# Kernel tuning notes

Hardware: AMD Instinct MI355X
Metric: run time of the kernel (lower is better)

The kernel has to match this reference:

```python
import jax, jax.numpy as jnp
import numpy as np

NPOINT = 1024
RADIUS = 0.2
NSAMPLE = 32


def setup_inputs() -> dict:
    key = jax.random.key(0)
    ks = jax.random.split(key, 8)
    B, N, C = 8, 8192, 64
    xyz = jax.random.uniform(ks[0], (B, N, 3), dtype=jnp.float32)
    features = jax.random.normal(ks[1], (B, N, C), dtype=jnp.float32)
    c_in = C + 3  # QueryAndGroup concatenates relative xyz with features
    s = 0.05
    w1 = jax.random.normal(ks[2], (c_in, 64), dtype=jnp.float32) * s
    b1 = jnp.zeros((64,), jnp.float32)
    w2 = jax.random.normal(ks[3], (64, 64), dtype=jnp.float32) * s
    b2 = jnp.zeros((64,), jnp.float32)
    w3 = jax.random.normal(ks[4], (64, 128), dtype=jnp.float32) * s
    b3 = jnp.zeros((128,), jnp.float32)
    return {"xyz": xyz, "features": features, "w1": w1, "b1": b1,
            "w2": w2, "b2": b2, "w3": w3, "b3": b3}


def farthest_point_sample(xyz, npoint):
    # xyz: (B, N, 3) -> (B, npoint) int32 indices
    B, N, _ = xyz.shape

    def step(carry, _):
        dist, far = carry
        centroid = jnp.take_along_axis(xyz, far[:, None, None], axis=1)  # (B,1,3)
        d = jnp.sum((xyz - centroid) ** 2, axis=-1)  # (B,N)
        dist = jnp.minimum(dist, d)
        nxt = jnp.argmax(dist, axis=-1).astype(jnp.int32)
        return (dist, nxt), far

    init = (jnp.full((B, N), 1e10, jnp.float32), jnp.zeros((B,), jnp.int32))
    _, idxs = jax.lax.scan(step, init, None, length=npoint)
    return idxs.T  # (B, npoint)


def ball_query(radius, nsample, xyz, new_xyz):
    # returns (B, S, nsample) int32 neighbor indices into N
    sq = jnp.sum((new_xyz[:, :, None, :] - xyz[:, None, :, :]) ** 2, axis=-1)  # (B,S,N)
    B, S, N = sq.shape
    idx = jnp.broadcast_to(jnp.arange(N, dtype=jnp.int32), (B, S, N))
    idx = jnp.where(sq > radius * radius, N, idx)
    idx = jnp.sort(idx, axis=-1)[:, :, :nsample]
    first = idx[:, :, :1]
    idx = jnp.where(idx == N, first, idx)  # pad with first valid index
    return idx


_gather = jax.vmap(lambda pts, idx: pts[idx])  # per-batch fancy gather


def reference(xyz, features, w1, b1, w2, b2, w3, b3):
    fps_idx = farthest_point_sample(xyz, NPOINT)
    new_xyz = _gather(xyz, fps_idx)  # (B, S, 3)
    nbr_idx = ball_query(RADIUS, NSAMPLE, xyz, new_xyz)  # (B, S, K)
    g_xyz = _gather(xyz, nbr_idx) - new_xyz[:, :, None, :]  # (B,S,K,3) relative coords
    g_feat = _gather(features, nbr_idx)  # (B, S, K, C)
    x = jnp.concatenate([g_xyz, g_feat], axis=-1)  # (B, S, K, C+3)
    # shared pointwise MLP (Conv2d 1x1 + ReLU)
    x = jax.nn.relu(x @ w1 + b1)
    x = jax.nn.relu(x @ w2 + b2)
    x = jax.nn.relu(x @ w3 + b3)
    new_features = jnp.max(x, axis=2)  # max-pool over neighbors -> (B, S, 128)
    return new_xyz, jnp.transpose(new_features, (0, 2, 1))  # (B,S,3), (B,128,S)
```

## Files before the change

### kernel.cpp

```cpp
#include <hip/hip_runtime.h>
#include <stdint.h>

#define N_PTS 8192
#define B_SZ 8
#define NPOINT_ 1024
#define NSAMPLE_ 32

typedef float __attribute__((ext_vector_type(2))) f32x2;

template <int CTRL>
__device__ __forceinline__ float dpp_maxf(float v) {
    int o = __builtin_amdgcn_update_dpp(__float_as_int(v), __float_as_int(v),
                                        CTRL, 0xf, 0xf, false);
    return fmaxf(v, __int_as_float(o));
}
template <int CTRL>
__device__ __forceinline__ int dpp_mini(int v) {
    int o = __builtin_amdgcn_update_dpp(v, v, CTRL, 0xf, 0xf, false);
    return (o < v) ? o : v;
}

__global__ __launch_bounds__(512) void fps_kernel(const float* __restrict__ xyz,
                                                  float* __restrict__ new_xyz) {
    __shared__ float4 spts[N_PTS];
    __shared__ float  cval[2][8];
    __shared__ int    cidx[2][8];
    const int b = blockIdx.x;
    const int t = threadIdx.x;
    const float* bx = xyz + (size_t)b * N_PTS * 3;

    f32x2 px[8], py[8], pz[8], dst[8];
#pragma unroll
    for (int jj = 0; jj < 8; ++jj) {
        int p0 = t + 512 * (2 * jj);
        int p1 = t + 512 * (2 * jj + 1);
        float x0 = bx[3 * p0 + 0], y0 = bx[3 * p0 + 1], z0 = bx[3 * p0 + 2];
        float x1 = bx[3 * p1 + 0], y1 = bx[3 * p1 + 1], z1 = bx[3 * p1 + 2];
        spts[p0] = make_float4(x0, y0, z0, 0.0f);
        spts[p1] = make_float4(x1, y1, z1, 0.0f);
        px[jj] = f32x2{x0, x1}; py[jj] = f32x2{y0, y1}; pz[jj] = f32x2{z0, z1};
        dst[jj] = f32x2{1e10f, 1e10f};
    }
    __syncthreads();

    float cx = bx[0], cy = bx[1], cz = bx[2];
    if (t == 0) {
        new_xyz[(b * NPOINT_) * 3 + 0] = cx;
        new_xyz[(b * NPOINT_) * 3 + 1] = cy;
        new_xyz[(b * NPOINT_) * 3 + 2] = cz;
    }
    const int wave = t >> 6, lane = t & 63;

    for (int it = 1; it < NPOINT_; ++it) {
        f32x2 cx2 = f32x2{cx, cx}, cy2 = f32x2{cy, cy}, cz2 = f32x2{cz, cz};
        {
#pragma clang fp contract(off)
#pragma unroll
            for (int jj = 0; jj < 8; ++jj) {
                f32x2 dx = px[jj] - cx2;
                f32x2 dy = py[jj] - cy2;
                f32x2 dz = pz[jj] - cz2;
                f32x2 d  = (dx * dx + dy * dy) + dz * dz;
                dst[jj] = __builtin_elementwise_min(dst[jj], d);
            }
        }
        f32x2 m01 = __builtin_elementwise_max(dst[0], dst[1]);
        f32x2 m23 = __builtin_elementwise_max(dst[2], dst[3]);
        f32x2 m45 = __builtin_elementwise_max(dst[4], dst[5]);
        f32x2 m67 = __builtin_elementwise_max(dst[6], dst[7]);
        f32x2 m03 = __builtin_elementwise_max(m01, m23);
        f32x2 m47 = __builtin_elementwise_max(m45, m67);
        f32x2 mm  = __builtin_elementwise_max(m03, m47);
        float bv  = fmaxf(mm.x, mm.y);
        int lj = 0;
#pragma unroll
        for (int jj = 7; jj >= 0; --jj) {
            lj = (dst[jj].y == bv) ? 2 * jj + 1 : lj;
            lj = (dst[jj].x == bv) ? 2 * jj     : lj;
        }
        int idx = (lj << 9) + t;

        float mv = bv;
        mv = dpp_maxf<0x111>(mv);
        mv = dpp_maxf<0x112>(mv);
        mv = dpp_maxf<0x114>(mv);
        mv = dpp_maxf<0x118>(mv);
        mv = dpp_maxf<0x142>(mv);
        mv = dpp_maxf<0x143>(mv);
        float wmax = __int_as_float(__builtin_amdgcn_readlane(__float_as_int(mv), 63));
        int ic = (bv == wmax) ? idx : 0x7FFFFFFF;
        ic = dpp_mini<0x111>(ic);
        ic = dpp_mini<0x112>(ic);
        ic = dpp_mini<0x114>(ic);
        ic = dpp_mini<0x118>(ic);
        ic = dpp_mini<0x142>(ic);
        ic = dpp_mini<0x143>(ic);

        const int buf = it & 1;
        if (lane == 63) { cval[buf][wave] = wmax; cidx[buf][wave] = ic; }
        __syncthreads();

        float cv = cval[buf][lane & 7];
        int   ci = cidx[buf][lane & 7];
        float gm = cv;
        gm = dpp_maxf<0x111>(gm);
        gm = dpp_maxf<0x112>(gm);
        gm = dpp_maxf<0x114>(gm);
        float gmax = __int_as_float(__builtin_amdgcn_readlane(__float_as_int(gm), 7));
        int ic2 = (cv == gmax) ? ci : 0x7FFFFFFF;
        ic2 = dpp_mini<0x111>(ic2);
        ic2 = dpp_mini<0x112>(ic2);
        ic2 = dpp_mini<0x114>(ic2);
        int wi = __builtin_amdgcn_readlane(ic2, 7);

        float4 sp = spts[wi];
        cx = sp.x; cy = sp.y; cz = sp.z;
        if (t == 0) {
            new_xyz[(b * NPOINT_ + it) * 3 + 0] = cx;
            new_xyz[(b * NPOINT_ + it) * 3 + 1] = cy;
            new_xyz[(b * NPOINT_ + it) * 3 + 2] = cz;
        }
    }
}

__global__ __launch_bounds__(512) void ballquery_kernel(const float* __restrict__ xyz,
                                                        const float* __restrict__ new_xyz,
                                                        int* __restrict__ nbr_idx) {
    __shared__ float sx[N_PTS], sy[N_PTS], sz[N_PTS];
    const int b     = blockIdx.x >> 4;
    const int chunk = blockIdx.x & 15;
    const int t = threadIdx.x;
    const float* bx = xyz + (size_t)b * N_PTS * 3;
    for (int p = t; p < N_PTS; p += 512) {
        sx[p] = bx[3 * p + 0];
        sy[p] = bx[3 * p + 1];
        sz[p] = bx[3 * p + 2];
    }
    __syncthreads();
    const int wave = t >> 6, lane = t & 63;
    const float r2 = 0.04f;

    for (int si = 0; si < 8; ++si) {
        int s = chunk * 64 + wave * 8 + si;
        int g = b * NPOINT_ + s;
        float cx = new_xyz[g * 3 + 0];
        float cy = new_xyz[g * 3 + 1];
        float cz = new_xyz[g * 3 + 2];
        int taken = 0;
        int firstIdx = -1;
        int* ob = nbr_idx + (size_t)g * NSAMPLE_;
        for (int c = 0; c < N_PTS / 64 && taken < NSAMPLE_; ++c) {
            int p = c * 64 + lane;
            float dx = __fsub_rn(sx[p], cx);
            float dy = __fsub_rn(sy[p], cy);
            float dz = __fsub_rn(sz[p], cz);
            float sq = __fadd_rn(__fadd_rn(__fmul_rn(dx, dx), __fmul_rn(dy, dy)),
                                 __fmul_rn(dz, dz));
            bool pred = !(sq > r2);
            unsigned long long mask = __ballot(pred);
            if (mask) {
                int cnt = __popcll(mask);
                if (firstIdx < 0) firstIdx = c * 64 + (__ffsll(mask) - 1);
                if (pred) {
                    int pos = taken + __popcll(mask & ((1ull << lane) - 1ull));
                    if (pos < NSAMPLE_) ob[pos] = p;
                }
                taken += cnt;
            }
        }
        if (lane >= taken && lane < NSAMPLE_) ob[lane] = firstIdx;
    }
}

__global__ __launch_bounds__(512, 2) void mlp_kernel(const float* __restrict__ xyz,
                                                     const float* __restrict__ feat,
                                                     const float* __restrict__ new_xyz,
                                                     const int* __restrict__ nbr_idx,
                                                     const float* __restrict__ w1,
                                                     const float* __restrict__ b1,
                                                     const float* __restrict__ w2,
                                                     const float* __restrict__ b2,
                                                     const float* __restrict__ w3,
                                                     const float* __restrict__ b3,
                                                     float* __restrict__ out) {
    __shared__ float lw1T[64 * 68];
    __shared__ float lb1[64];
    __shared__ float lw2T[64 * 64];
    __shared__ float lb2[64];
    __shared__ float lw3T[128 * 64];
    __shared__ float lb3[128];
    __shared__ float xb[8][16 * 68];
    __shared__ float hb[8][16 * 68];

    const int t = threadIdx.x;
    for (int i = t; i < 67 * 64; i += 512) { int k = i >> 6, c = i & 63; lw1T[c * 68 + k] = w1[i]; }
    if (t < 64) lw1T[t * 68 + 67] = 0.0f;
    for (int i = t; i < 64 * 64; i += 512)  { int k = i >> 6, c = i & 63;  lw2T[c * 64 + k] = w2[i]; }
    for (int i = t; i < 64 * 128; i += 512) { int k = i >> 7, c = i & 127; lw3T[c * 64 + k] = w3[i]; }
    if (t < 64)  { lb1[t] = b1[t]; lb2[t] = b2[t]; }
    if (t < 128) lb3[t] = b3[t];
    __syncthreads();

    const int wave = t >> 6, lane = t & 63;
    float* xw = xb[wave];
    float* hw = hb[wave];
    const float* wc1 = lw1T + lane * 68;
    const float* wc2 = lw2T + lane * 64;
    const float* wca = lw3T + lane * 64;
    const float* wcb = lw3T + (lane + 64) * 64;

    for (int g = blockIdx.x * 8 + wave; g < B_SZ * NPOINT_; g += gridDim.x * 8) {
        const int b = g >> 10, s = g & 1023;
        const float cx = new_xyz[g * 3 + 0];
        const float cy = new_xyz[g * 3 + 1];
        const float cz = new_xyz[g * 3 + 2];
        float mo0 = 0.0f, mo1 = 0.0f;

        for (int half = 0; half < 2; ++half) {
            int iis[16];
#pragma unroll
            for (int r = 0; r < 16; ++r)
                iis[r] = nbr_idx[(size_t)g * NSAMPLE_ + half * 16 + r];
#pragma unroll
            for (int r = 0; r < 16; ++r) {
                xw[r * 68 + 3 + lane] = feat[((size_t)b * N_PTS + iis[r]) * 64 + lane];
                if (lane < 3) {
                    float pv = xyz[((size_t)b * N_PTS + iis[r]) * 3 + lane];
                    float cv = (lane == 0) ? cx : ((lane == 1) ? cy : cz);
                    xw[r * 68 + lane] = pv - cv;
                }
                if (lane == 0) xw[r * 68 + 67] = 0.0f;
            }
            f32x2 acc2[16];
            {
                float bias = lb1[lane];
#pragma unroll
                for (int r = 0; r < 16; ++r) acc2[r] = f32x2{bias, 0.0f};
                for (int kk = 0; kk < 68; kk += 4) {
                    f32x2 wA = *(const f32x2*)(wc1 + kk);
                    f32x2 wB = *(const f32x2*)(wc1 + kk + 2);
#pragma unroll
                    for (int r = 0; r < 16; ++r) {
                        float4 xv = *(const float4*)&xw[r * 68 + kk];
                        f32x2 xa = f32x2{xv.x, xv.y};
                        f32x2 xc = f32x2{xv.z, xv.w};
                        acc2[r] = xa * wA + acc2[r];
                        acc2[r] = xc * wB + acc2[r];
                    }
                }
#pragma unroll
                for (int r = 0; r < 16; ++r)
                    hw[r * 68 + lane] = fmaxf(acc2[r].x + acc2[r].y, 0.0f);
            }
            {
                float bias = lb2[lane];
#pragma unroll
                for (int r = 0; r < 16; ++r) acc2[r] = f32x2{bias, 0.0f};
                for (int kk = 0; kk < 64; kk += 4) {
                    f32x2 wA = *(const f32x2*)(wc2 + kk);
                    f32x2 wB = *(const f32x2*)(wc2 + kk + 2);
#pragma unroll
                    for (int r = 0; r < 16; ++r) {
                        float4 hv = *(const float4*)&hw[r * 68 + kk];
                        f32x2 xa = f32x2{hv.x, hv.y};
                        f32x2 xc = f32x2{hv.z, hv.w};
                        acc2[r] = xa * wA + acc2[r];
                        acc2[r] = xc * wB + acc2[r];
                    }
                }
#pragma unroll
                for (int r = 0; r < 16; ++r)
                    xw[r * 68 + lane] = fmaxf(acc2[r].x + acc2[r].y, 0.0f);
            }
            {
                f32x2 a2[16], c2[16];
                float bb0 = lb3[lane], bb1 = lb3[lane + 64];
#pragma unroll
                for (int r = 0; r < 16; ++r) { a2[r] = f32x2{bb0, 0.0f}; c2[r] = f32x2{bb1, 0.0f}; }
                for (int kk = 0; kk < 64; kk += 4) {
                    f32x2 wA0 = *(const f32x2*)(wca + kk);
                    f32x2 wB0 = *(const f32x2*)(wca + kk + 2);
                    f32x2 wA1 = *(const f32x2*)(wcb + kk);
                    f32x2 wB1 = *(const f32x2*)(wcb + kk + 2);
#pragma unroll
                    for (int r = 0; r < 16; ++r) {
                        float4 hv = *(const float4*)&xw[r * 68 + kk];
                        f32x2 xa = f32x2{hv.x, hv.y};
                        f32x2 xc = f32x2{hv.z, hv.w};
                        a2[r] = xa * wA0 + a2[r];
                        a2[r] = xc * wB0 + a2[r];
                        c2[r] = xa * wA1 + c2[r];
                        c2[r] = xc * wB1 + c2[r];
                    }
                }
#pragma unroll
                for (int r = 0; r < 16; ++r) {
                    mo0 = fmaxf(mo0, fmaxf(a2[r].x + a2[r].y, 0.0f));
                    mo1 = fmaxf(mo1, fmaxf(c2[r].x + c2[r].y, 0.0f));
                }
            }
        }
        out[((size_t)b * 128 + lane) * 1024 + s]      = mo0;
        out[((size_t)b * 128 + lane + 64) * 1024 + s] = mo1;
    }
}

extern "C" void kernel_launch(void* const* d_in, const int* in_sizes, int n_in,
                              void* d_out, int out_size, void* d_ws, size_t ws_size,
                              hipStream_t stream) {
    const float* xyz  = (const float*)d_in[0];
    const float* feat = (const float*)d_in[1];
    const float* w1   = (const float*)d_in[2];
    const float* b1   = (const float*)d_in[3];
    const float* w2   = (const float*)d_in[4];
    const float* b2   = (const float*)d_in[5];
    const float* w3   = (const float*)d_in[6];
    const float* b3   = (const float*)d_in[7];

    float* out_xyz  = (float*)d_out;
    float* out_feat = (float*)d_out + B_SZ * NPOINT_ * 3;
    int*   nbr      = (int*)d_ws;

    fps_kernel<<<B_SZ, 512, 0, stream>>>(xyz, out_xyz);
    ballquery_kernel<<<B_SZ * 16, 512, 0, stream>>>(xyz, out_xyz, nbr);
    mlp_kernel<<<256, 512, 0, stream>>>(xyz, feat, out_xyz, nbr,
                                        w1, b1, w2, b2, w3, b3, out_feat);
}
```

Baseline: 1.234 ms.

## Fuse FPS, ball query and MLP into one producer-consumer persistent kernel

Replaces the three launches with one kernel. Eight producer blocks run farthest-point sampling and publish a progress counter every 64 centroids, while consumer blocks spin-wait on that counter and then run the ball query and MLP per centroid. This overlaps the serial FPS with the downstream work and drops the neighbor-index round trip through global memory. In exchange, ball query now reads xyz from global memory instead of LDS. Correctness depends on all producer blocks being co-resident with the consumers, otherwise the spin-wait can deadlock.

Measured after the change: 1.026 ms. 16.9% less time.

```diff
diff --git a/kernel.cpp b/kernel.cpp
--- a/kernel.cpp
+++ b/kernel.cpp
@@ -5,6 +5,10 @@
 #define B_SZ 8
 #define NPOINT_ 1024
 #define NSAMPLE_ 32
+#define NPROD 8
+#define NCONS 240
+#define CWAVES (NCONS * 8)
+#define PUBK 64
 
 typedef float __attribute__((ext_vector_type(2))) f32x2;
 
@@ -20,309 +24,347 @@
     return (o < v) ? o : v;
 }
 
-__global__ __launch_bounds__(512) void fps_kernel(const float* __restrict__ xyz,
-                                                  float* __restrict__ new_xyz) {
-    __shared__ float4 spts[N_PTS];
-    __shared__ float  cval[2][8];
-    __shared__ int    cidx[2][8];
-    const int b = blockIdx.x;
+__device__ __forceinline__ float ld_coh(const float* p) {
+    return __int_as_float(__hip_atomic_load((int*)p, __ATOMIC_RELAXED,
+                                            __HIP_MEMORY_SCOPE_AGENT));
+}
+__device__ __forceinline__ void st_coh(float* p, float v) {
+    __hip_atomic_store((int*)p, __float_as_int(v), __ATOMIC_RELAXED,
+                       __HIP_MEMORY_SCOPE_AGENT);
+}
+
+#define SM_SPTS 0
+#define SM_CVAL 131072
+#define SM_CIDX 131136
+#define SM_W1 0
+#define SM_W2 17408
+#define SM_W3 33792
+#define SM_B1 66560
+#define SM_B2 66816
+#define SM_B3 67072
+#define SM_XB 67584
+#define SM_HB 102400
+#define SM_NIDX 137216
+#define SM_TOTAL 138240
+
+__global__ __launch_bounds__(512, 2) void fused_kernel(
+    const float* __restrict__ xyz, const float* __restrict__ feat,
+    const float* __restrict__ w1, const float* __restrict__ b1,
+    const float* __restrict__ w2, const float* __restrict__ b2,
+    const float* __restrict__ w3, const float* __restrict__ b3,
+    float* __restrict__ new_xyz, float* __restrict__ out,
+    int* __restrict__ prog) {
+    __shared__ __align__(16) char smem[SM_TOTAL];
     const int t = threadIdx.x;
-    const float* bx = xyz + (size_t)b * N_PTS * 3;
-
-    f32x2 px[8], py[8], pz[8], dst[8];
-#pragma unroll
-    for (int jj = 0; jj < 8; ++jj) {
-        int p0 = t + 512 * (2 * jj);
-        int p1 = t + 512 * (2 * jj + 1);
-        float x0 = bx[3 * p0 + 0], y0 = bx[3 * p0 + 1], z0 = bx[3 * p0 + 2];
-        float x1 = bx[3 * p1 + 0], y1 = bx[3 * p1 + 1], z1 = bx[3 * p1 + 2];
-        spts[p0] = make_float4(x0, y0, z0, 0.0f);
-        spts[p1] = make_float4(x1, y1, z1, 0.0f);
-        px[jj] = f32x2{x0, x1}; py[jj] = f32x2{y0, y1}; pz[jj] = f32x2{z0, z1};
-        dst[jj] = f32x2{1e10f, 1e10f};
+    const int wave = t >> 6, lane = t & 63;
+
+    if (blockIdx.x < NPROD) {
+        float4* spts = (float4*)smem;
+        float* cval = (float*)(smem + SM_CVAL);
+        int* cidx = (int*)(smem + SM_CIDX);
+        const int b = blockIdx.x;
+        const float* bx = xyz + (size_t)b * N_PTS * 3;
+        int* pp = prog + b * 64;
+
+        f32x2 px[8], py[8], pz[8], dst[8];
+#pragma unroll
+        for (int jj = 0; jj < 8; ++jj) {
+            int p0 = t + 512 * (2 * jj);
+            int p1 = t + 512 * (2 * jj + 1);
+            float x0 = bx[3 * p0 + 0], y0 = bx[3 * p0 + 1], z0 = bx[3 * p0 + 2];
+            float x1 = bx[3 * p1 + 0], y1 = bx[3 * p1 + 1], z1 = bx[3 * p1 + 2];
+            spts[p0] = make_float4(x0, y0, z0, 0.0f);
+            spts[p1] = make_float4(x1, y1, z1, 0.0f);
+            px[jj] = f32x2{x0, x1};
+            py[jj] = f32x2{y0, y1};
+            pz[jj] = f32x2{z0, z1};
+            dst[jj] = f32x2{1e10f, 1e10f};
+        }
+        __syncthreads();
+
+        float cx = bx[0], cy = bx[1], cz = bx[2];
+        if (t == 0) {
+            st_coh(&new_xyz[(b * NPOINT_) * 3 + 0], cx);
+            st_coh(&new_xyz[(b * NPOINT_) * 3 + 1], cy);
+            st_coh(&new_xyz[(b * NPOINT_) * 3 + 2], cz);
+        }
+
+        for (int it = 1; it < NPOINT_; ++it) {
+            f32x2 cx2 = f32x2{cx, cx}, cy2 = f32x2{cy, cy}, cz2 = f32x2{cz, cz};
+            {
+#pragma clang fp contract(off)
+#pragma unroll
+                for (int jj = 0; jj < 8; ++jj) {
+                    f32x2 dx = px[jj] - cx2;
+                    f32x2 dy = py[jj] - cy2;
+                    f32x2 dz = pz[jj] - cz2;
+                    f32x2 d = (dx * dx + dy * dy) + dz * dz;
+                    dst[jj] = __builtin_elementwise_min(dst[jj], d);
+                }
+            }
+            f32x2 m01 = __builtin_elementwise_max(dst[0], dst[1]);
+            f32x2 m23 = __builtin_elementwise_max(dst[2], dst[3]);
+            f32x2 m45 = __builtin_elementwise_max(dst[4], dst[5]);
+            f32x2 m67 = __builtin_elementwise_max(dst[6], dst[7]);
+            f32x2 m03 = __builtin_elementwise_max(m01, m23);
+            f32x2 m47 = __builtin_elementwise_max(m45, m67);
+            f32x2 mm = __builtin_elementwise_max(m03, m47);
+            float bv = fmaxf(mm.x, mm.y);
+            int lj = 0;
+#pragma unroll
+            for (int jj = 7; jj >= 0; --jj) {
+                lj = (dst[jj].y == bv) ? 2 * jj + 1 : lj;
+                lj = (dst[jj].x == bv) ? 2 * jj : lj;
+            }
+            int idx = (lj << 9) + t;
+
+            float mv = bv;
+            mv = dpp_maxf<0x111>(mv);
+            mv = dpp_maxf<0x112>(mv);
+            mv = dpp_maxf<0x114>(mv);
+            mv = dpp_maxf<0x118>(mv);
+            mv = dpp_maxf<0x142>(mv);
+            mv = dpp_maxf<0x143>(mv);
+            float wmax = __int_as_float(
+                __builtin_amdgcn_readlane(__float_as_int(mv), 63));
+            int ic = (bv == wmax) ? idx : 0x7FFFFFFF;
+            ic = dpp_mini<0x111>(ic);
+            ic = dpp_mini<0x112>(ic);
+            ic = dpp_mini<0x114>(ic);
+            ic = dpp_mini<0x118>(ic);
+            ic = dpp_mini<0x142>(ic);
+            ic = dpp_mini<0x143>(ic);
+
+            const int buf = it & 1;
+            if (lane == 63) {
+                cval[buf * 8 + wave] = wmax;
+                cidx[buf * 8 + wave] = ic;
+            }
+            __syncthreads();
+
+            float cv = cval[buf * 8 + (lane & 7)];
+            int ci = cidx[buf * 8 + (lane & 7)];
+            float gm = cv;
+            gm = dpp_maxf<0x111>(gm);
+            gm = dpp_maxf<0x112>(gm);
+            gm = dpp_maxf<0x114>(gm);
+            float gmax =
+                __int_as_float(__builtin_amdgcn_readlane(__float_as_int(gm), 7));
+            int ic2 = (cv == gmax) ? ci : 0x7FFFFFFF;
+            ic2 = dpp_mini<0x111>(ic2);
+            ic2 = dpp_mini<0x112>(ic2);
+            ic2 = dpp_mini<0x114>(ic2);
+            int wi = __builtin_amdgcn_readlane(ic2, 7);
+
+            float4 sp = spts[wi];
+            cx = sp.x;
+            cy = sp.y;
+            cz = sp.z;
+            if (t == 0) {
+                st_coh(&new_xyz[(b * NPOINT_ + it) * 3 + 0], cx);
+                st_coh(&new_xyz[(b * NPOINT_ + it) * 3 + 1], cy);
+                st_coh(&new_xyz[(b * NPOINT_ + it) * 3 + 2], cz);
+                if ((it & (PUBK - 1)) == (PUBK - 1)) {
+                    __hip_atomic_store(pp, it + 1, __ATOMIC_RELEASE,
+                                       __HIP_MEMORY_SCOPE_AGENT);
+                }
+            }
+        }
+    } else {
+        float* lw1T = (float*)(smem + SM_W1);
+        float* lw2T = (float*)(smem + SM_W2);
+        float* lw3T = (float*)(smem + SM_W3);
+        float* lb1 = (float*)(smem + SM_B1);
+        float* lb2 = (float*)(smem + SM_B2);
+        float* lb3 = (float*)(smem + SM_B3);
+
+        for (int i = t; i < 67 * 64; i += 512) {
+            int k = i >> 6, c = i & 63;
+            lw1T[c * 68 + k] = w1[i];
+        }
+        if (t < 64) lw1T[t * 68 + 67] = 0.0f;
+        for (int i = t; i < 64 * 64; i += 512) {
+            int k = i >> 6, c = i & 63;
+            lw2T[c * 64 + k] = w2[i];
+        }
+        for (int i = t; i < 64 * 128; i += 512) {
+            int k = i >> 7, c = i & 127;
+            lw3T[c * 64 + k] = w3[i];
+        }
+        if (t < 64) {
+            lb1[t] = b1[t];
+            lb2[t] = b2[t];
+        }
+        if (t < 128) lb3[t] = b3[t];
+        __syncthreads();
+
+        float* xw = (float*)(smem + SM_XB) + wave * (16 * 68);
+        float* hw = (float*)(smem + SM_HB) + wave * (16 * 68);
+        int* nw = (int*)(smem + SM_NIDX) + wave * 32;
+        const float* wc1 = lw1T + lane * 68;
+        const float* wc2 = lw2T + lane * 64;
+        const float* wca = lw3T + lane * 64;
+        const float* wcb = lw3T + (lane + 64) * 64;
+
+        const int widx = (blockIdx.x - NPROD) * 8 + wave;
+        for (int cc = widx; cc < B_SZ * NPOINT_; cc += CWAVES) {
+            const int s = cc >> 3, b = cc & 7;
+            const int g = (b << 10) + s;
+            int* pp = prog + b * 64;
+
+            int pv = __hip_atomic_load(pp, __ATOMIC_RELAXED,
+                                       __HIP_MEMORY_SCOPE_AGENT);
+            while (pv <= s) {
+                if (s - pv >= 64)
+                    __builtin_amdgcn_s_sleep(64);
+                else
+                    __builtin_amdgcn_s_sleep(16);
+                pv = __hip_atomic_load(pp, __ATOMIC_RELAXED,
+                                       __HIP_MEMORY_SCOPE_AGENT);
+            }
+            __builtin_amdgcn_fence(__ATOMIC_ACQUIRE, "agent");
+            const float cx = ld_coh(&new_xyz[g * 3 + 0]);
+            const float cy = ld_coh(&new_xyz[g * 3 + 1]);
+            const float cz = ld_coh(&new_xyz[g * 3 + 2]);
+
+            const float* bx = xyz + (size_t)b * N_PTS * 3;
+            const float r2 = 0.04f;
+            int taken = 0, firstIdx = -1;
+            for (int ch = 0; ch < N_PTS / 64 && taken < NSAMPLE_; ++ch) {
+                int p = ch * 64 + lane;
+                float dxq = __fsub_rn(bx[3 * p + 0], cx);
+                float dyq = __fsub_rn(bx[3 * p + 1], cy);
+                float dzq = __fsub_rn(bx[3 * p + 2], cz);
+                float sq = __fadd_rn(
+                    __fadd_rn(__fmul_rn(dxq, dxq), __fmul_rn(dyq, dyq)),
+                    __fmul_rn(dzq, dzq));
+                bool pred = !(sq > r2);
+                unsigned long long mask = __ballot(pred);
+                if (mask) {
+                    int cnt = __popcll(mask);
+                    if (firstIdx < 0) firstIdx = ch * 64 + (__ffsll(mask) - 1);
+                    if (pred) {
+                        int pos =
+                            taken + __popcll(mask & ((1ull << lane) - 1ull));
+                        if (pos < NSAMPLE_) nw[pos] = p;
+                    }
+                    taken += cnt;
+                }
+            }
+            if (lane >= taken && lane < NSAMPLE_) nw[lane] = firstIdx;
+            asm volatile("s_waitcnt lgkmcnt(0)" ::: "memory");
+
+            float mo0 = 0.0f, mo1 = 0.0f;
+            for (int half = 0; half < 2; ++half) {
+                int iis[16];
+#pragma unroll
+                for (int r = 0; r < 16; ++r) iis[r] = nw[half * 16 + r];
+#pragma unroll
+                for (int r = 0; r < 16; ++r) {
+                    xw[r * 68 + 3 + lane] =
+                        feat[((size_t)b * N_PTS + iis[r]) * 64 + lane];
+                    if (lane < 3) {
+                        float pv2 = xyz[((size_t)b * N_PTS + iis[r]) * 3 + lane];
+                        float cv = (lane == 0) ? cx : ((lane == 1) ? cy : cz);
+                        xw[r * 68 + lane] = pv2 - cv;
+                    }
+                    if (lane == 0) xw[r * 68 + 67] = 0.0f;
+                }
+                f32x2 acc2[16];
+                {
+                    float bias = lb1[lane];
+#pragma unroll
+                    for (int r = 0; r < 16; ++r) acc2[r] = f32x2{bias, 0.0f};
+                    for (int kk = 0; kk < 68; kk += 4) {
+                        f32x2 wA = *(const f32x2*)(wc1 + kk);
+                        f32x2 wB = *(const f32x2*)(wc1 + kk + 2);
+#pragma unroll
+                        for (int r = 0; r < 16; ++r) {
+                            float4 xv = *(const float4*)&xw[r * 68 + kk];
+                            f32x2 xa = f32x2{xv.x, xv.y};
+                            f32x2 xc = f32x2{xv.z, xv.w};
+                            acc2[r] = xa * wA + acc2[r];
+                            acc2[r] = xc * wB + acc2[r];
+                        }
+                    }
+#pragma unroll
+                    for (int r = 0; r < 16; ++r)
+                        hw[r * 68 + lane] = fmaxf(acc2[r].x + acc2[r].y, 0.0f);
+                }
+                {
+                    float bias = lb2[lane];
+#pragma unroll
+                    for (int r = 0; r < 16; ++r) acc2[r] = f32x2{bias, 0.0f};
+                    for (int kk = 0; kk < 64; kk += 4) {
+                        f32x2 wA = *(const f32x2*)(wc2 + kk);
+                        f32x2 wB = *(const f32x2*)(wc2 + kk + 2);
+#pragma unroll
+                        for (int r = 0; r < 16; ++r) {
+                            float4 hv = *(const float4*)&hw[r * 68 + kk];
+                            f32x2 xa = f32x2{hv.x, hv.y};
+                            f32x2 xc = f32x2{hv.z, hv.w};
+                            acc2[r] = xa * wA + acc2[r];
+                            acc2[r] = xc * wB + acc2[r];
+                        }
+                    }
+#pragma unroll
+                    for (int r = 0; r < 16; ++r)
+                        xw[r * 68 + lane] = fmaxf(acc2[r].x + acc2[r].y, 0.0f);
+                }
+                {
+                    f32x2 a2[16], c2[16];
+                    float bb0 = lb3[lane], bb1 = lb3[lane + 64];
+#pragma unroll
+                    for (int r = 0; r < 16; ++r) {
+                        a2[r] = f32x2{bb0, 0.0f};
+                        c2[r] = f32x2{bb1, 0.0f};
+                    }
+                    for (int kk = 0; kk < 64; kk += 4) {
+                        f32x2 wA0 = *(const f32x2*)(wca + kk);
+                        f32x2 wB0 = *(const f32x2*)(wca + kk + 2);
+                        f32x2 wA1 = *(const f32x2*)(wcb + kk);
+                        f32x2 wB1 = *(const f32x2*)(wcb + kk + 2);
+#pragma unroll
+                        for (int r = 0; r < 16; ++r) {
+                            float4 hv = *(const float4*)&xw[r * 68 + kk];
+                            f32x2 xa = f32x2{hv.x, hv.y};
+                            f32x2 xc = f32x2{hv.z, hv.w};
+                            a2[r] = xa * wA0 + a2[r];
+                            a2[r] = xc * wB0 + a2[r];
+                            c2[r] = xa * wA1 + c2[r];
+                            c2[r] = xc * wB1 + c2[r];
+                        }
+                    }
+#pragma unroll
+                    for (int r = 0; r < 16; ++r) {
+                        mo0 = fmaxf(mo0, fmaxf(a2[r].x + a2[r].y, 0.0f));
+                        mo1 = fmaxf(mo1, fmaxf(c2[r].x + c2[r].y, 0.0f));
+                    }
+                }
+            }
+            out[((size_t)b * 128 + lane) * 1024 + s] = mo0;
+            out[((size_t)b * 128 + lane + 64) * 1024 + s] = mo1;
+        }
     }
-    __syncthreads();
-
-    float cx = bx[0], cy = bx[1], cz = bx[2];
-    if (t == 0) {
-        new_xyz[(b * NPOINT_) * 3 + 0] = cx;
-        new_xyz[(b * NPOINT_) * 3 + 1] = cy;
-        new_xyz[(b * NPOINT_) * 3 + 2] = cz;
-    }
-    const int wave = t >> 6, lane = t & 63;
-
-    for (int it = 1; it < NPOINT_; ++it) {
-        f32x2 cx2 = f32x2{cx, cx}, cy2 = f32x2{cy, cy}, cz2 = f32x2{cz, cz};
-        {
-#pragma clang fp contract(off)
-#pragma unroll
-            for (int jj = 0; jj < 8; ++jj) {
-                f32x2 dx = px[jj] - cx2;
-                f32x2 dy = py[jj] - cy2;
-                f32x2 dz = pz[jj] - cz2;
-                f32x2 d  = (dx * dx + dy * dy) + dz * dz;
-                dst[jj] = __builtin_elementwise_min(dst[jj], d);
-            }
-        }
-        f32x2 m01 = __builtin_elementwise_max(dst[0], dst[1]);
-        f32x2 m23 = __builtin_elementwise_max(dst[2], dst[3]);
-        f32x2 m45 = __builtin_elementwise_max(dst[4], dst[5]);
-        f32x2 m67 = __builtin_elementwise_max(dst[6], dst[7]);
-        f32x2 m03 = __builtin_elementwise_max(m01, m23);
-        f32x2 m47 = __builtin_elementwise_max(m45, m67);
-        f32x2 mm  = __builtin_elementwise_max(m03, m47);
-        float bv  = fmaxf(mm.x, mm.y);
-        int lj = 0;
-#pragma unroll
-        for (int jj = 7; jj >= 0; --jj) {
-            lj = (dst[jj].y == bv) ? 2 * jj + 1 : lj;
-            lj = (dst[jj].x == bv) ? 2 * jj     : lj;
-        }
-        int idx = (lj << 9) + t;
-
-        float mv = bv;
-        mv = dpp_maxf<0x111>(mv);
-        mv = dpp_maxf<0x112>(mv);
-        mv = dpp_maxf<0x114>(mv);
-        mv = dpp_maxf<0x118>(mv);
-        mv = dpp_maxf<0x142>(mv);
-        mv = dpp_maxf<0x143>(mv);
-        float wmax = __int_as_float(__builtin_amdgcn_readlane(__float_as_int(mv), 63));
-        int ic = (bv == wmax) ? idx : 0x7FFFFFFF;
-        ic = dpp_mini<0x111>(ic);
-        ic = dpp_mini<0x112>(ic);
-        ic = dpp_mini<0x114>(ic);
-        ic = dpp_mini<0x118>(ic);
-        ic = dpp_mini<0x142>(ic);
-        ic = dpp_mini<0x143>(ic);
-
-        const int buf = it & 1;
-        if (lane == 63) { cval[buf][wave] = wmax; cidx[buf][wave] = ic; }
-        __syncthreads();
-
-        float cv = cval[buf][lane & 7];
-        int   ci = cidx[buf][lane & 7];
-        float gm = cv;
-        gm = dpp_maxf<0x111>(gm);
-        gm = dpp_maxf<0x112>(gm);
-        gm = dpp_maxf<0x114>(gm);
-        float gmax = __int_as_float(__builtin_amdgcn_readlane(__float_as_int(gm), 7));
-        int ic2 = (cv == gmax) ? ci : 0x7FFFFFFF;
-        ic2 = dpp_mini<0x111>(ic2);
-        ic2 = dpp_mini<0x112>(ic2);
-        ic2 = dpp_mini<0x114>(ic2);
-        int wi = __builtin_amdgcn_readlane(ic2, 7);
-
-        float4 sp = spts[wi];
-        cx = sp.x; cy = sp.y; cz = sp.z;
-        if (t == 0) {
-            new_xyz[(b * NPOINT_ + it) * 3 + 0] = cx;
-            new_xyz[(b * NPOINT_ + it) * 3 + 1] = cy;
-            new_xyz[(b * NPOINT_ + it) * 3 + 2] = cz;
-        }
-    }
-}
-
-__global__ __launch_bounds__(512) void ballquery_kernel(const float* __restrict__ xyz,
-                                                        const float* __restrict__ new_xyz,
-                                                        int* __restrict__ nbr_idx) {
-    __shared__ float sx[N_PTS], sy[N_PTS], sz[N_PTS];
-    const int b     = blockIdx.x >> 4;
-    const int chunk = blockIdx.x & 15;
-    const int t = threadIdx.x;
-    const float* bx = xyz + (size_t)b * N_PTS * 3;
-    for (int p = t; p < N_PTS; p += 512) {
-        sx[p] = bx[3 * p + 0];
-        sy[p] = bx[3 * p + 1];
-        sz[p] = bx[3 * p + 2];
-    }
-    __syncthreads();
-    const int wave = t >> 6, lane = t & 63;
-    const float r2 = 0.04f;
-
-    for (int si = 0; si < 8; ++si) {
-        int s = chunk * 64 + wave * 8 + si;
-        int g = b * NPOINT_ + s;
-        float cx = new_xyz[g * 3 + 0];
-        float cy = new_xyz[g * 3 + 1];
-        float cz = new_xyz[g * 3 + 2];
-        int taken = 0;
-        int firstIdx = -1;
-        int* ob = nbr_idx + (size_t)g * NSAMPLE_;
-        for (int c = 0; c < N_PTS / 64 && taken < NSAMPLE_; ++c) {
-            int p = c * 64 + lane;
-            float dx = __fsub_rn(sx[p], cx);
-            float dy = __fsub_rn(sy[p], cy);
-            float dz = __fsub_rn(sz[p], cz);
-            float sq = __fadd_rn(__fadd_rn(__fmul_rn(dx, dx), __fmul_rn(dy, dy)),
-                                 __fmul_rn(dz, dz));
-            bool pred = !(sq > r2);
-            unsigned long long mask = __ballot(pred);
-            if (mask) {
-                int cnt = __popcll(mask);
-                if (firstIdx < 0) firstIdx = c * 64 + (__ffsll(mask) - 1);
-                if (pred) {
-                    int pos = taken + __popcll(mask & ((1ull << lane) - 1ull));
-                    if (pos < NSAMPLE_) ob[pos] = p;
-                }
-                taken += cnt;
-            }
-        }
-        if (lane >= taken && lane < NSAMPLE_) ob[lane] = firstIdx;
-    }
-}
-
-__global__ __launch_bounds__(512, 2) void mlp_kernel(const float* __restrict__ xyz,
-                                                     const float* __restrict__ feat,
-                                                     const float* __restrict__ new_xyz,
-                                                     const int* __restrict__ nbr_idx,
-                                                     const float* __restrict__ w1,
-                                                     const float* __restrict__ b1,
-                                                     const float* __restrict__ w2,
-                                                     const float* __restrict__ b2,
-                                                     const float* __restrict__ w3,
-                                                     const float* __restrict__ b3,
-                                                     float* __restrict__ out) {
-    __shared__ float lw1T[64 * 68];
-    __shared__ float lb1[64];
-    __shared__ float lw2T[64 * 64];
-    __shared__ float lb2[64];
-    __shared__ float lw3T[128 * 64];
-    __shared__ float lb3[128];
-    __shared__ float xb[8][16 * 68];
-    __shared__ float hb[8][16 * 68];
-
-    const int t = threadIdx.x;
-    for (int i = t; i < 67 * 64; i += 512) { int k = i >> 6, c = i & 63; lw1T[c * 68 + k] = w1[i]; }
-    if (t < 64) lw1T[t * 68 + 67] = 0.0f;
-    for (int i = t; i < 64 * 64; i += 512)  { int k = i >> 6, c = i & 63;  lw2T[c * 64 + k] = w2[i]; }
-    for (int i = t; i < 64 * 128; i += 512) { int k = i >> 7, c = i & 127; lw3T[c * 64 + k] = w3[i]; }
-    if (t < 64)  { lb1[t] = b1[t]; lb2[t] = b2[t]; }
-    if (t < 128) lb3[t] = b3[t];
-    __syncthreads();
-
-    const int wave = t >> 6, lane = t & 63;
-    float* xw = xb[wave];
-    float* hw = hb[wave];
-    const float* wc1 = lw1T + lane * 68;
-    const float* wc2 = lw2T + lane * 64;
-    const float* wca = lw3T + lane * 64;
-    const float* wcb = lw3T + (lane + 64) * 64;
-
-    for (int g = blockIdx.x * 8 + wave; g < B_SZ * NPOINT_; g += gridDim.x * 8) {
-        const int b = g >> 10, s = g & 1023;
-        const float cx = new_xyz[g * 3 + 0];
-        const float cy = new_xyz[g * 3 + 1];
-        const float cz = new_xyz[g * 3 + 2];
-        float mo0 = 0.0f, mo1 = 0.0f;
-
-        for (int half = 0; half < 2; ++half) {
-            int iis[16];
-#pragma unroll
-            for (int r = 0; r < 16; ++r)
-                iis[r] = nbr_idx[(size_t)g * NSAMPLE_ + half * 16 + r];
-#pragma unroll
-            for (int r = 0; r < 16; ++r) {
-                xw[r * 68 + 3 + lane] = feat[((size_t)b * N_PTS + iis[r]) * 64 + lane];
-                if (lane < 3) {
-                    float pv = xyz[((size_t)b * N_PTS + iis[r]) * 3 + lane];
-                    float cv = (lane == 0) ? cx : ((lane == 1) ? cy : cz);
-                    xw[r * 68 + lane] = pv - cv;
-                }
-                if (lane == 0) xw[r * 68 + 67] = 0.0f;
-            }
-            f32x2 acc2[16];
-            {
-                float bias = lb1[lane];
-#pragma unroll
-                for (int r = 0; r < 16; ++r) acc2[r] = f32x2{bias, 0.0f};
-                for (int kk = 0; kk < 68; kk += 4) {
-                    f32x2 wA = *(const f32x2*)(wc1 + kk);
-                    f32x2 wB = *(const f32x2*)(wc1 + kk + 2);
-#pragma unroll
-                    for (int r = 0; r < 16; ++r) {
-                        float4 xv = *(const float4*)&xw[r * 68 + kk];
-                        f32x2 xa = f32x2{xv.x, xv.y};
-                        f32x2 xc = f32x2{xv.z, xv.w};
-                        acc2[r] = xa * wA + acc2[r];
-                        acc2[r] = xc * wB + acc2[r];
-                    }
-                }
-#pragma unroll
-                for (int r = 0; r < 16; ++r)
-                    hw[r * 68 + lane] = fmaxf(acc2[r].x + acc2[r].y, 0.0f);
-            }
-            {
-                float bias = lb2[lane];
-#pragma unroll
-                for (int r = 0; r < 16; ++r) acc2[r] = f32x2{bias, 0.0f};
-                for (int kk = 0; kk < 64; kk += 4) {
-                    f32x2 wA = *(const f32x2*)(wc2 + kk);
-                    f32x2 wB = *(const f32x2*)(wc2 + kk + 2);
-#pragma unroll
-                    for (int r = 0; r < 16; ++r) {
-                        float4 hv = *(const float4*)&hw[r * 68 + kk];
-                        f32x2 xa = f32x2{hv.x, hv.y};
-                        f32x2 xc = f32x2{hv.z, hv.w};
-                        acc2[r] = xa * wA + acc2[r];
-                        acc2[r] = xc * wB + acc2[r];
-                    }
-                }
-#pragma unroll
-                for (int r = 0; r < 16; ++r)
-                    xw[r * 68 + lane] = fmaxf(acc2[r].x + acc2[r].y, 0.0f);
-            }
-            {
-                f32x2 a2[16], c2[16];
-                float bb0 = lb3[lane], bb1 = lb3[lane + 64];
-#pragma unroll
-                for (int r = 0; r < 16; ++r) { a2[r] = f32x2{bb0, 0.0f}; c2[r] = f32x2{bb1, 0.0f}; }
-                for (int kk = 0; kk < 64; kk += 4) {
-                    f32x2 wA0 = *(const f32x2*)(wca + kk);
-                    f32x2 wB0 = *(const f32x2*)(wca + kk + 2);
-                    f32x2 wA1 = *(const f32x2*)(wcb + kk);
-                    f32x2 wB1 = *(const f32x2*)(wcb + kk + 2);
-#pragma unroll
-                    for (int r = 0; r < 16; ++r) {
-                        float4 hv = *(const float4*)&xw[r * 68 + kk];
-                        f32x2 xa = f32x2{hv.x, hv.y};
-                        f32x2 xc = f32x2{hv.z, hv.w};
-                        a2[r] = xa * wA0 + a2[r];
-                        a2[r] = xc * wB0 + a2[r];
-                        c2[r] = xa * wA1 + c2[r];
-                        c2[r] = xc * wB1 + c2[r];
-                    }
-                }
-#pragma unroll
-                for (int r = 0; r < 16; ++r) {
-                    mo0 = fmaxf(mo0, fmaxf(a2[r].x + a2[r].y, 0.0f));
-                    mo1 = fmaxf(mo1, fmaxf(c2[r].x + c2[r].y, 0.0f));
-                }
-            }
-        }
-        out[((size_t)b * 128 + lane) * 1024 + s]      = mo0;
-        out[((size_t)b * 128 + lane + 64) * 1024 + s] = mo1;
-    }
 }
 
 extern "C" void kernel_launch(void* const* d_in, const int* in_sizes, int n_in,
-                              void* d_out, int out_size, void* d_ws, size_t ws_size,
-                              hipStream_t stream) {
-    const float* xyz  = (const float*)d_in[0];
+                              void* d_out, int out_size, void* d_ws,
+                              size_t ws_size, hipStream_t stream) {
+    const float* xyz = (const float*)d_in[0];
     const float* feat = (const float*)d_in[1];
-    const float* w1   = (const float*)d_in[2];
-    const float* b1   = (const float*)d_in[3];
-    const float* w2   = (const float*)d_in[4];
-    const float* b2   = (const float*)d_in[5];
-    const float* w3   = (const float*)d_in[6];
-    const float* b3   = (const float*)d_in[7];
-
-    float* out_xyz  = (float*)d_out;
+    const float* w1 = (const float*)d_in[2];
+    const float* b1 = (const float*)d_in[3];
+    const float* w2 = (const float*)d_in[4];
+    const float* b2 = (const float*)d_in[5];
+    const float* w3 = (const float*)d_in[6];
+    const float* b3 = (const float*)d_in[7];
+
+    float* out_xyz = (float*)d_out;
     float* out_feat = (float*)d_out + B_SZ * NPOINT_ * 3;
-    int*   nbr      = (int*)d_ws;
-
-    fps_kernel<<<B_SZ, 512, 0, stream>>>(xyz, out_xyz);
-    ballquery_kernel<<<B_SZ * 16, 512, 0, stream>>>(xyz, out_xyz, nbr);
-    mlp_kernel<<<256, 512, 0, stream>>>(xyz, feat, out_xyz, nbr,
-                                        w1, b1, w2, b2, w3, b3, out_feat);
-}
+    int* prog = (int*)d_ws;
+
+    hipMemsetAsync(d_ws, 0, NPROD * 64 * sizeof(int), stream);
+    fused_kernel<<<NPROD + NCONS, 512, 0, stream>>>(
+        xyz, feat, w1, b1, w2, b2, w3, b3, out_xyz, out_feat, prog);
+}
```
